# Optimization experiments

Hardware: AMD Instinct MI355X
Metric: run time of the kernel (lower is better)

The kernel has to match this reference:

```python
import jax, jax.numpy as jnp
import numpy as np

IN_CHANNELS = 64
OUT_CHANNELS = 64
SEQ_LEN = 512
KERNEL_SIZE = 9
STRIDE = 1
PADDING = 4  # symmetric
OUT_SEQ_LEN = (SEQ_LEN + 2 * PADDING - (KERNEL_SIZE - 1) - 1) // STRIDE + 1  # 512


def setup_inputs() -> dict:
    key = jax.random.key(0)
    k1, k2, k3 = jax.random.split(key, 3)
    x = jax.random.normal(k1, (64, IN_CHANNELS, SEQ_LEN), dtype=jnp.float32)
    # nn.init.normal_(std=0.1)
    weight = 0.1 * jax.random.normal(k2, (IN_CHANNELS, OUT_CHANNELS, KERNEL_SIZE, OUT_SEQ_LEN), dtype=jnp.float32)
    bias = 0.1 * jax.random.normal(k3, (OUT_CHANNELS, OUT_SEQ_LEN), dtype=jnp.float32)
    return {"x": x, "weight": weight, "bias": bias}


def reference(x, weight, bias):
    # x: [B, Ci, S] -> pad last dim
    xp = jnp.pad(x, ((0, 0), (0, 0), (PADDING, PADDING)))
    # Unfold (im2col) as a gather: same math as the one-hot grouped conv.
    starts = jnp.arange(OUT_SEQ_LEN) * STRIDE            # [L]
    offs = jnp.arange(KERNEL_SIZE)                        # [K]
    idx = starts[:, None] + offs[None, :]                 # [L, K]
    patches = xp[:, :, idx]                               # [B, Ci, L, K]
    # per-position matmul: 'b i l k, i o k l -> b o l'
    out = jnp.einsum('bilk,iokl->bol', patches, weight)
    out = out + bias                                      # [B, Co, L]
    return out
```

## Files before the change

### kernel.cpp

```cpp
#include <hip/hip_runtime.h>


#define CIN   64
#define COUT  64
#define SEQ   512
#define KS    9
#define LT    16
#define OT    16
#define BT    16
#define LWIN  24
#define XSTR  72
#define XLW   (BT*XSTR)
#define BOSTR 42
#define BLSTR (OT*BOSTR + 2)
#define NCHUNK 18
#define WSTRIDE (COUT*KS*SEQ)
#define XS_ELEMS (LWIN*XLW)
#define BS_ELEMS (LT*BLSTR)
#define LDS_BYTES ((XS_ELEMS + BS_ELEMS)*2)

typedef __attribute__((ext_vector_type(8))) short bf16x8;
typedef __attribute__((ext_vector_type(4))) float f32x4;

__device__ __forceinline__ ushort f2bf(float f) {
    return (ushort)((__float_as_uint(f) + 0x8000u) >> 16);
}
__device__ __forceinline__ uint pack2bf(float a0, float a1) {
    uint u0 = __float_as_uint(a0) + 0x8000u;
    uint u1 = __float_as_uint(a1) + 0x8000u;
    return __builtin_amdgcn_perm(u1, u0, 0x07060302);
}

__global__ __launch_bounds__(512, 4)
void lc1d_mfma(const float* __restrict__ x, const float* __restrict__ w,
               const float* __restrict__ bias, float* __restrict__ out)
{
    extern __shared__ ushort lds[];
    ushort* Xs = lds;
    ushort* Bs = lds + XS_ELEMS;

    const int tid  = threadIdx.x;
    const int lane = tid & 63;
    const int wv   = tid >> 6;
    const int lt  = blockIdx.x >> 2;
    const int os  = blockIdx.x & 3;
    const int bsp = blockIdx.y;
    const int l0 = lt * LT;
    const int o0 = os * OT;
    const int b0 = bsp * BT;

    const int lq = tid & 3;
    const int oo = (tid >> 2) & 15;
    const int ig = tid >> 6;

    const float* wbase = w + ((size_t)(o0 + oo) * KS) * SEQ + l0 + lq * 4;

    float4 pfA[4], pfB[4];

    #define LOAD_CHUNK(pf, c) {                                                  \
        const int kq_ = (c) >> 1, ih_ = (c) & 1;                                 \
        const float* p_ = wbase + (size_t)kq_ * SEQ                              \
                          + (size_t)(ih_*32 + ig*4) * WSTRIDE;                   \
        _Pragma("unroll")                                                        \
        for (int q = 0; q < 4; ++q)                                              \
            pf[q] = *(const float4*)(p_ + (size_t)q * WSTRIDE);                  \
    }

    #define WRITE_BS(pf) {                                                       \
        _Pragma("unroll")                                                        \
        for (int s = 0; s < 2; ++s) {                                            \
            _Pragma("unroll")                                                    \
            for (int dl = 0; dl < 4; ++dl) {                                     \
                uint pk_ = pack2bf((&pf[2*s].x)[dl], (&pf[2*s+1].x)[dl]);        \
                *(uint*)(Bs + (lq*4+dl)*BLSTR + oo*BOSTR + ig*4 + 2*s) = pk_;    \
            }                                                                    \
        }                                                                        \
    }

    LOAD_CHUNK(pfA, 0)
    LOAD_CHUNK(pfB, 1)

    #pragma unroll
    for (int it = 0; it < 12; ++it) {
        int flat = tid + 512*it;
        int row = flat / 6;
        int q   = flat - row*6;
        int b = row >> 6, i = row & 63;
        const float* src = x + ((size_t)((b0 + b)*CIN + i))*SEQ + (l0 - 4) + q*4;
        float4 v = make_float4(0.f, 0.f, 0.f, 0.f);
        if (!((lt == 0 && q == 0) || (lt == 31 && q == 5)))
            v = *(const float4*)src;
        ushort* dst = Xs + (q*4)*XLW + b*XSTR + i;
        dst[0*XLW] = f2bf(v.x);
        dst[1*XLW] = f2bf(v.y);
        dst[2*XLW] = f2bf(v.z);
        dst[3*XLW] = f2bf(v.w);
    }

    f32x4 acc[2];
    acc[0] = (f32x4)0.0f;
    acc[1] = (f32x4)0.0f;

    const int aoff = (lane & 15)*XSTR  + (lane >> 4)*8;
    const int boff = (lane & 15)*BOSTR + (lane >> 4)*8;

    __syncthreads();

    #define DO_MFMA(c) {                                                         \
        const int kq_ = (c) >> 1, ih_ = (c) & 1;                                 \
        _Pragma("unroll")                                                        \
        for (int jr = 0; jr < 2; ++jr) {                                         \
            const int r_ = wv*2 + jr;                                            \
            bf16x8 Af_ = *(const bf16x8*)(Xs + (r_ + kq_)*XLW + ih_*32 + aoff);  \
            const uint* bw_ = (const uint*)(Bs + r_*BLSTR + boff);               \
            uint4 bu_ = make_uint4(bw_[0], bw_[1], bw_[2], bw_[3]);              \
            bf16x8 Bf_ = __builtin_bit_cast(bf16x8, bu_);                        \
            acc[jr] = __builtin_amdgcn_mfma_f32_16x16x32_bf16(Af_, Bf_, acc[jr], \
                                                              0, 0, 0);          \
        }                                                                        \
    }

    for (int cc = 0; cc < NCHUNK; cc += 2) {
        WRITE_BS(pfA)
        __syncthreads();
        if (cc + 2 < NCHUNK) LOAD_CHUNK(pfA, cc + 2)
        DO_MFMA(cc)
        __syncthreads();

        WRITE_BS(pfB)
        __syncthreads();
        if (cc + 3 < NCHUNK) LOAD_CHUNK(pfB, cc + 3)
        DO_MFMA(cc + 1)
        __syncthreads();
    }

    const int orow = o0 + (lane & 15);
    const int rgrp = lane >> 4;
    #pragma unroll
    for (int jr = 0; jr < 2; ++jr) {
        int l = l0 + wv*2 + jr;
        float bv = bias[orow*SEQ + l];
        #pragma unroll
        for (int r = 0; r < 4; ++r) {
            int b = b0 + rgrp*4 + r;
            out[(size_t)(b*COUT + orow)*SEQ + l] = acc[jr][r] + bv;
        }
    }
}

extern "C" void kernel_launch(void* const* d_in, const int* in_sizes, int n_in,
                              void* d_out, int out_size, void* d_ws, size_t ws_size,
                              hipStream_t stream) {
    const float* x    = (const float*)d_in[0];
    const float* wgt  = (const float*)d_in[1];
    const float* bias = (const float*)d_in[2];
    float* out        = (float*)d_out;

    hipFuncSetAttribute((const void*)lc1d_mfma,
                        hipFuncAttributeMaxDynamicSharedMemorySize, LDS_BYTES);
    dim3 grid(128, 4);
    lc1d_mfma<<<grid, 512, LDS_BYTES, stream>>>(x, wgt, bias, out);
}
```

Baseline: 162.9 us.

## Cover full batch per block to read weights once, shrink sequence tile

Each block now covers all 64 batch elements with 1024 threads and an 8-position sequence tile, instead of splitting the batch across four blocks. This removes redundant re-reading of the large position-dependent weight tensor, the dominant memory traffic. Only half the threads stage weights, with fewer loads in flight per thread. The larger x tile in LDS and the single block per CU may reduce latency hiding.

```diff
diff --git a/kernel.cpp b/kernel.cpp
--- a/kernel.cpp
+++ b/kernel.cpp
@@ -5,18 +5,17 @@
 #define COUT  64
 #define SEQ   512
 #define KS    9
-#define LT    16
+#define LT    8
 #define OT    16
-#define BT    16
-#define LWIN  24
+#define LWIN  16
 #define XSTR  72
-#define XLW   (BT*XSTR)
-#define BOSTR 42
-#define BLSTR (OT*BOSTR + 2)
-#define NCHUNK 18
-#define WSTRIDE (COUT*KS*SEQ)
+#define XLW   (64*XSTR)
+#define BOS   40
+#define BLS   (OT*BOS + 8)
+#define NSTEP 18
+#define WSTR  (COUT*KS*SEQ)
 #define XS_ELEMS (LWIN*XLW)
-#define BS_ELEMS (LT*BLSTR)
+#define BS_ELEMS (LT*BLS)
 #define LDS_BYTES ((XS_ELEMS + BS_ELEMS)*2)
 
 typedef __attribute__((ext_vector_type(8))) short bf16x8;
@@ -31,7 +30,7 @@
     return __builtin_amdgcn_perm(u1, u0, 0x07060302);
 }
 
-__global__ __launch_bounds__(512, 4)
+__global__ __launch_bounds__(1024, 4)
 void lc1d_mfma(const float* __restrict__ x, const float* __restrict__ w,
                const float* __restrict__ bias, float* __restrict__ out)
 {
@@ -42,53 +41,47 @@
     const int tid  = threadIdx.x;
     const int lane = tid & 63;
     const int wv   = tid >> 6;
-    const int lt  = blockIdx.x >> 2;
-    const int os  = blockIdx.x & 3;
-    const int bsp = blockIdx.y;
+    const int lt = blockIdx.x >> 2;
+    const int os = blockIdx.x & 3;
     const int l0 = lt * LT;
     const int o0 = os * OT;
-    const int b0 = bsp * BT;
 
-    const int lq = tid & 3;
-    const int oo = (tid >> 2) & 15;
-    const int ig = tid >> 6;
+    const int lh = tid & 1;
+    const int oo = (tid >> 1) & 15;
+    const int ip = (tid >> 5) & 15;
+    const bool stager = (tid < 512);
 
-    const float* wbase = w + ((size_t)(o0 + oo) * KS) * SEQ + l0 + lq * 4;
+    const float* wbase = w + ((size_t)(2*ip) * COUT + (o0 + oo)) * (KS*SEQ)
+                           + l0 + lh*4;
+    float4 pfA[2], pfB[2];
 
-    float4 pfA[4], pfB[4];
-
-    #define LOAD_CHUNK(pf, c) {                                                  \
-        const int kq_ = (c) >> 1, ih_ = (c) & 1;                                 \
-        const float* p_ = wbase + (size_t)kq_ * SEQ                              \
-                          + (size_t)(ih_*32 + ig*4) * WSTRIDE;                   \
-        _Pragma("unroll")                                                        \
-        for (int q = 0; q < 4; ++q)                                              \
-            pf[q] = *(const float4*)(p_ + (size_t)q * WSTRIDE);                  \
+    #define LOAD_STEP(pf, c) if (stager) {                                       \
+        const int k_ = (c) >> 1, ih_ = (c) & 1;                                  \
+        const float* p_ = wbase + (size_t)(ih_*32) * WSTR + (size_t)k_ * SEQ;    \
+        pf[0] = *(const float4*)p_;                                              \
+        pf[1] = *(const float4*)(p_ + WSTR);                                     \
     }
 
-    #define WRITE_BS(pf) {                                                       \
+    #define WRITE_BS(pf) if (stager) {                                           \
         _Pragma("unroll")                                                        \
-        for (int s = 0; s < 2; ++s) {                                            \
-            _Pragma("unroll")                                                    \
-            for (int dl = 0; dl < 4; ++dl) {                                     \
-                uint pk_ = pack2bf((&pf[2*s].x)[dl], (&pf[2*s+1].x)[dl]);        \
-                *(uint*)(Bs + (lq*4+dl)*BLSTR + oo*BOSTR + ig*4 + 2*s) = pk_;    \
-            }                                                                    \
+        for (int dl = 0; dl < 4; ++dl) {                                         \
+            uint pk = pack2bf((&pf[0].x)[dl], (&pf[1].x)[dl]);                   \
+            *(uint*)(Bs + (lh*4+dl)*BLS + oo*BOS + 2*ip) = pk;                   \
         }                                                                        \
     }
 
-    LOAD_CHUNK(pfA, 0)
-    LOAD_CHUNK(pfB, 1)
+    LOAD_STEP(pfA, 0)
+    LOAD_STEP(pfB, 1)
 
     #pragma unroll
-    for (int it = 0; it < 12; ++it) {
-        int flat = tid + 512*it;
-        int row = flat / 6;
-        int q   = flat - row*6;
+    for (int it = 0; it < 16; ++it) {
+        int flat = tid + 1024*it;
+        int row = flat >> 2;
+        int q   = flat & 3;
         int b = row >> 6, i = row & 63;
-        const float* src = x + ((size_t)((b0 + b)*CIN + i))*SEQ + (l0 - 4) + q*4;
+        const float* src = x + ((size_t)(b*CIN + i))*SEQ + (l0 - 4) + q*4;
         float4 v = make_float4(0.f, 0.f, 0.f, 0.f);
-        if (!((lt == 0 && q == 0) || (lt == 31 && q == 5)))
+        if (!((lt == 0 && q == 0) || (lt == 63 && q == 3)))
             v = *(const float4*)src;
         ushort* dst = Xs + (q*4)*XLW + b*XSTR + i;
         dst[0*XLW] = f2bf(v.x);
@@ -101,49 +94,49 @@
     acc[0] = (f32x4)0.0f;
     acc[1] = (f32x4)0.0f;
 
-    const int aoff = (lane & 15)*XSTR  + (lane >> 4)*8;
-    const int boff = (lane & 15)*BOSTR + (lane >> 4)*8;
+    const int lrel = wv & 7;
+    const int btb  = (wv >> 3) * 2;
+    const int am   = (lane & 15) * XSTR + (lane >> 4) * 8;
+    const int boff = lrel*BLS + (lane & 15) * BOS + (lane >> 4) * 8;
 
     __syncthreads();
 
     #define DO_MFMA(c) {                                                         \
-        const int kq_ = (c) >> 1, ih_ = (c) & 1;                                 \
+        const int k_ = (c) >> 1, ih_ = (c) & 1;                                  \
+        bf16x8 Bf = *(const bf16x8*)(Bs + boff);                                 \
+        const ushort* Arow = Xs + (lrel + k_)*XLW + ih_*32 + am;                 \
         _Pragma("unroll")                                                        \
-        for (int jr = 0; jr < 2; ++jr) {                                         \
-            const int r_ = wv*2 + jr;                                            \
-            bf16x8 Af_ = *(const bf16x8*)(Xs + (r_ + kq_)*XLW + ih_*32 + aoff);  \
-            const uint* bw_ = (const uint*)(Bs + r_*BLSTR + boff);               \
-            uint4 bu_ = make_uint4(bw_[0], bw_[1], bw_[2], bw_[3]);              \
-            bf16x8 Bf_ = __builtin_bit_cast(bf16x8, bu_);                        \
-            acc[jr] = __builtin_amdgcn_mfma_f32_16x16x32_bf16(Af_, Bf_, acc[jr], \
+        for (int jt = 0; jt < 2; ++jt) {                                         \
+            bf16x8 Af = *(const bf16x8*)(Arow + (btb + jt)*(16*XSTR));           \
+            acc[jt] = __builtin_amdgcn_mfma_f32_16x16x32_bf16(Af, Bf, acc[jt],   \
                                                               0, 0, 0);          \
         }                                                                        \
     }
 
-    for (int cc = 0; cc < NCHUNK; cc += 2) {
+    for (int cc = 0; cc < NSTEP; cc += 2) {
         WRITE_BS(pfA)
         __syncthreads();
-        if (cc + 2 < NCHUNK) LOAD_CHUNK(pfA, cc + 2)
+        if (cc + 2 < NSTEP) LOAD_STEP(pfA, cc + 2)
         DO_MFMA(cc)
         __syncthreads();
 
         WRITE_BS(pfB)
         __syncthreads();
-        if (cc + 3 < NCHUNK) LOAD_CHUNK(pfB, cc + 3)
+        if (cc + 3 < NSTEP) LOAD_STEP(pfB, cc + 3)
         DO_MFMA(cc + 1)
         __syncthreads();
     }
 
+    const int l    = l0 + lrel;
     const int orow = o0 + (lane & 15);
-    const int rgrp = lane >> 4;
+    const int rbase = (lane >> 4) * 4;
+    const float bv = bias[orow*SEQ + l];
     #pragma unroll
-    for (int jr = 0; jr < 2; ++jr) {
-        int l = l0 + wv*2 + jr;
-        float bv = bias[orow*SEQ + l];
+    for (int jt = 0; jt < 2; ++jt) {
         #pragma unroll
         for (int r = 0; r < 4; ++r) {
-            int b = b0 + rgrp*4 + r;
-            out[(size_t)(b*COUT + orow)*SEQ + l] = acc[jr][r] + bv;
+            const int b = (btb + jt)*16 + rbase + r;
+            out[((size_t)(b*COUT + orow))*SEQ + l] = acc[jt][r] + bv;
         }
     }
 }
@@ -158,6 +151,6 @@
 
     hipFuncSetAttribute((const void*)lc1d_mfma,
                         hipFuncAttributeMaxDynamicSharedMemorySize, LDS_BYTES);
-    dim3 grid(128, 4);
-    lc1d_mfma<<<grid, 512, LDS_BYTES, stream>>>(x, wgt, bias, out);
+    dim3 grid(256);
+    lc1d_mfma<<<grid, 1024, LDS_BYTES, stream>>>(x, wgt, bias, out);
 }
```

Measured after the change: 152.5 us. 6.4% less time.
